# Kernel optimization log

Measured on AMD Instinct MI355X. Metric: run time of the kernel, lower is better.

## Reference

```python
import jax, jax.numpy as jnp
import numpy as np

BLOCK_SIZE = 256
EMB = 384
HEAD = 64
B = 256
T = 256

def setup_inputs() -> dict:
    key = jax.random.key(0)
    k1, k2, k3, k4 = jax.random.split(key, 4)
    x = jax.random.normal(k1, (B, T, EMB), dtype=jnp.float32)
    # torch Linear(no bias) default init ~ U(-1/sqrt(in), 1/sqrt(in)); use scaled normal
    s = 1.0 / np.sqrt(EMB)
    Wq = jax.random.normal(k2, (EMB, HEAD), dtype=jnp.float32) * s
    Wk = jax.random.normal(k3, (EMB, HEAD), dtype=jnp.float32) * s
    Wv = jax.random.normal(k4, (EMB, HEAD), dtype=jnp.float32) * s
    return {"x": x, "Wq": Wq, "Wk": Wk, "Wv": Wv}

def reference(x, Wq, Wk, Wv):
    Bb, Tt, C = x.shape
    q = jnp.einsum('btc,ch->bth', x, Wq)
    k = jnp.einsum('btc,ch->bth', x, Wk)
    v = jnp.einsum('btc,ch->bth', x, Wv)
    # NOTE: source scales by C**-0.5 where C = embedding dim (384), not head_size
    scores = jnp.einsum('bth,bsh->bts', q, k) * (C ** -0.5)  # [B,T,T]
    causal = jnp.tril(jnp.ones((Tt, Tt), dtype=bool))
    scores = jnp.where(causal, scores, -jnp.inf)
    weights = jax.nn.softmax(scores, axis=-1)
    # dropout is identity in eval mode (reference baseline)
    out = jnp.einsum('bts,bsh->bth', weights, v)
    return out
```

## Files before the change

kernel.cpp:

```cpp
#include <hip/hip_runtime.h>
#include <hip/hip_bf16.h>
#include <cstdint>
#include <cstddef>

#define B_DIM 256
#define T_DIM 256
#define EMB   384
#define HEAD  64
#define QS    (B_DIM * T_DIM * HEAD)

typedef __attribute__((ext_vector_type(8))) short bf16x8;
typedef __attribute__((ext_vector_type(4))) float f32x4;
typedef __attribute__((ext_vector_type(4))) unsigned int u32x4;

__device__ __forceinline__ unsigned short f2bf(float f) {
    union { float f; unsigned int u; } v; v.f = f;
    unsigned int r = v.u + 0x7fffu + ((v.u >> 16) & 1u);
    return (unsigned short)(r >> 16);
}

__global__ void wprep_kernel(const float* __restrict__ Wq, const float* __restrict__ Wk,
                             const float* __restrict__ Wv, unsigned short* __restrict__ Wb) {
    int idx = blockIdx.x * blockDim.x + threadIdx.x;
    if (idx >= 192 * EMB) return;
    int n = idx / EMB, k = idx - n * EMB;
    const float* W = (n < 64) ? Wq : (n < 128) ? Wk : Wv;
    Wb[idx] = f2bf(W[k * HEAD + (n & 63)]);
}

__global__ __launch_bounds__(256) void qkv_kernel(const float* __restrict__ x,
                                                  const unsigned short* __restrict__ Wb,
                                                  unsigned short* __restrict__ qkv) {
    __shared__ unsigned short Xs[64][72];
    __shared__ unsigned short Ws[192][72];
    const int tid = threadIdx.x;
    const int w = tid >> 6, lane = tid & 63, qd = lane >> 4, l15 = lane & 15;
    const int m0 = blockIdx.x * 64;

    f32x4 acc[4][3];
#pragma unroll
    for (int mt = 0; mt < 4; ++mt)
#pragma unroll
        for (int nt = 0; nt < 3; ++nt) acc[mt][nt] = (f32x4){0.f, 0.f, 0.f, 0.f};

    for (int kk = 0; kk < EMB; kk += 64) {
#pragma unroll
        for (int s = 0; s < 4; ++s) {
            int i = tid + 256 * s;
            int row = i >> 4, c4 = (i & 15) << 2;
            const float4 vx = *(const float4*)(x + (size_t)(m0 + row) * EMB + kk + c4);
            unsigned int lo = (unsigned)f2bf(vx.x) | ((unsigned)f2bf(vx.y) << 16);
            unsigned int hi = (unsigned)f2bf(vx.z) | ((unsigned)f2bf(vx.w) << 16);
            *(uint2*)&Xs[row][c4] = make_uint2(lo, hi);
        }
#pragma unroll
        for (int s = 0; s < 6; ++s) {
            int i = tid + 256 * s;
            int row = i >> 3, ch = (i & 7) << 3;
            *(u32x4*)&Ws[row][ch] = *(const u32x4*)(Wb + row * EMB + kk + ch);
        }
        __syncthreads();
#pragma unroll
        for (int kb = 0; kb < 2; ++kb) {
            bf16x8 a[4], bb[3];
#pragma unroll
            for (int mt = 0; mt < 4; ++mt)
                a[mt] = *(const bf16x8*)&Xs[16 * mt + l15][32 * kb + 8 * qd];
#pragma unroll
            for (int nt = 0; nt < 3; ++nt)
                bb[nt] = *(const bf16x8*)&Ws[48 * w + 16 * nt + l15][32 * kb + 8 * qd];
#pragma unroll
            for (int mt = 0; mt < 4; ++mt)
#pragma unroll
                for (int nt = 0; nt < 3; ++nt)
                    acc[mt][nt] = __builtin_amdgcn_mfma_f32_16x16x32_bf16(a[mt], bb[nt], acc[mt][nt], 0, 0, 0);
        }
        __syncthreads();
    }
#pragma unroll
    for (int nt = 0; nt < 3; ++nt) {
        int n = 48 * w + 16 * nt + l15;
        int arr = n >> 6, h = n & 63;
        unsigned short* dst = qkv + (size_t)arr * QS + h;
#pragma unroll
        for (int mt = 0; mt < 4; ++mt)
#pragma unroll
            for (int reg = 0; reg < 4; ++reg) {
                int row = m0 + 16 * mt + 4 * qd + reg;
                dst[(size_t)row * HEAD] = f2bf(acc[mt][nt][reg]);
            }
    }
}

__global__ __launch_bounds__(256, 1) void attn_kernel(const unsigned short* __restrict__ qkv,
                                                      float* __restrict__ out) {
    __shared__ unsigned short ks[256][72];
    __shared__ unsigned short vT[64][264];
    __shared__ unsigned short Ps[4][16][72];
    const int tid = threadIdx.x;
    const int w = tid >> 6, lane = tid & 63, qd = lane >> 4, l15 = lane & 15;
    const int b = blockIdx.x;
    const unsigned short* qb = qkv + (size_t)b * T_DIM * HEAD;
    const unsigned short* kb = qkv + (size_t)QS + (size_t)b * T_DIM * HEAD;
    const unsigned short* vb = qkv + 2 * (size_t)QS + (size_t)b * T_DIM * HEAD;

#pragma unroll
    for (int s = 0; s < 8; ++s) {
        int i = tid + 256 * s;
        int row = i >> 3, ch = (i & 7) << 3;
        *(u32x4*)&ks[row][ch] = *(const u32x4*)(kb + row * HEAD + ch);
    }
#pragma unroll
    for (int s = 0; s < 4; ++s) {
        int i = tid + 256 * s;
        int t = i >> 2, d0 = (i & 3) << 4;
        union { u32x4 v; unsigned short u[8]; } t0, t1;
        t0.v = *(const u32x4*)(vb + t * HEAD + d0);
        t1.v = *(const u32x4*)(vb + t * HEAD + d0 + 8);
#pragma unroll
        for (int e = 0; e < 8; ++e) { vT[d0 + e][t] = t0.u[e]; vT[d0 + 8 + e][t] = t1.u[e]; }
    }
    bf16x8 aq[4][2];
#pragma unroll
    for (int mt = 0; mt < 4; ++mt)
#pragma unroll
        for (int kbi = 0; kbi < 2; ++kbi)
            aq[mt][kbi] = *(const bf16x8*)(qb + (64 * mt + 16 * w + l15) * HEAD + 32 * kbi + 8 * qd);
    __syncthreads();

    f32x4 O[4][4];
    float l[4][4];
#pragma unroll
    for (int mt = 0; mt < 4; ++mt)
#pragma unroll
        for (int dn = 0; dn < 4; ++dn) O[mt][dn] = (f32x4){0.f, 0.f, 0.f, 0.f};
#pragma unroll
    for (int mt = 0; mt < 4; ++mt)
#pragma unroll
        for (int reg = 0; reg < 4; ++reg) l[mt][reg] = 0.f;

    const float cExp = 1.4426950408889634f / 19.595917942265423f;

    for (int mt = 0; mt < 4; ++mt) {
        for (int j = 0; j <= mt; ++j) {
            const int ntmax = (j == mt) ? w : 3;
            f32x4 S[4];
#pragma unroll
            for (int nt = 0; nt < 4; ++nt) {
                if (nt <= ntmax) {
                    bf16x8 b0 = *(const bf16x8*)&ks[64 * j + 16 * nt + l15][8 * qd];
                    bf16x8 b1 = *(const bf16x8*)&ks[64 * j + 16 * nt + l15][32 + 8 * qd];
                    f32x4 s = __builtin_amdgcn_mfma_f32_16x16x32_bf16(aq[mt][0], b0, (f32x4){0.f,0.f,0.f,0.f}, 0, 0, 0);
                    s = __builtin_amdgcn_mfma_f32_16x16x32_bf16(aq[mt][1], b1, s, 0, 0, 0);
                    S[nt] = s;
                }
            }
#pragma unroll
            for (int nt = 0; nt < 4; ++nt) {
#pragma unroll
                for (int reg = 0; reg < 4; ++reg) {
                    float p = 0.0f;
                    if (nt <= ntmax) {
                        p = exp2f(S[nt][reg] * cExp);
                        if (j == mt && nt == w && (l15 > 4 * qd + reg)) p = 0.0f;
                    }
                    l[mt][reg] += p;
                    Ps[w][4 * qd + reg][16 * nt + l15] = f2bf(p);
                }
            }
            bf16x8 ap0 = *(const bf16x8*)&Ps[w][l15][8 * qd];
            bf16x8 ap1 = *(const bf16x8*)&Ps[w][l15][32 + 8 * qd];
#pragma unroll
            for (int dn = 0; dn < 4; ++dn) {
                bf16x8 bv0 = *(const bf16x8*)&vT[16 * dn + l15][64 * j + 8 * qd];
                bf16x8 bv1 = *(const bf16x8*)&vT[16 * dn + l15][64 * j + 32 + 8 * qd];
                O[mt][dn] = __builtin_amdgcn_mfma_f32_16x16x32_bf16(ap0, bv0, O[mt][dn], 0, 0, 0);
                O[mt][dn] = __builtin_amdgcn_mfma_f32_16x16x32_bf16(ap1, bv1, O[mt][dn], 0, 0, 0);
            }
        }
    }

#pragma unroll
    for (int mt = 0; mt < 4; ++mt) {
#pragma unroll
        for (int reg = 0; reg < 4; ++reg) {
            float s = l[mt][reg];
            s += __shfl_xor(s, 1);
            s += __shfl_xor(s, 2);
            s += __shfl_xor(s, 4);
            s += __shfl_xor(s, 8);
            float inv = 1.0f / s;
            int row = 64 * mt + 16 * w + 4 * qd + reg;
            float* dst = out + ((size_t)b * T_DIM + row) * HEAD;
#pragma unroll
            for (int dn = 0; dn < 4; ++dn)
                dst[16 * dn + l15] = O[mt][dn][reg] * inv;
        }
    }
}

extern "C" void kernel_launch(void* const* d_in, const int* in_sizes, int n_in,
                              void* d_out, int out_size, void* d_ws, size_t ws_size,
                              hipStream_t stream) {
    const float* x  = (const float*)d_in[0];
    const float* Wq = (const float*)d_in[1];
    const float* Wk = (const float*)d_in[2];
    const float* Wv = (const float*)d_in[3];
    float* out = (float*)d_out;

    unsigned short* qkv = (unsigned short*)d_ws;
    unsigned short* Wb  = qkv + 3 * (size_t)QS;

    wprep_kernel<<<(192 * EMB + 255) / 256, 256, 0, stream>>>(Wq, Wk, Wv, Wb);
    qkv_kernel<<<(B_DIM * T_DIM) / 64, 256, 0, stream>>>(x, Wb, qkv);
    attn_kernel<<<B_DIM, 256, 0, stream>>>(qkv, out);
}
```

Baseline: 194.2 us.

## Enlarge QKV tiles with direct-to-LDS weight loads and balance causal attention across 8 waves

The QKV projection now computes 128 rows per block, with each wave owning a 64x96 output tile. Pre-swizzled bf16 weights are loaded straight into LDS via global_load_lds, and x is converted with a packed bf16 instruction. The attention kernel moves to 512 threads, and each wave handles query tiles w and 15-w so the causal work is balanced across waves. The goal is more reuse per block, fewer conversion instructions and better wave parallelism in attention, at the cost of higher register pressure from 24 accumulators and a new LDS swizzle layout.

```diff
diff --git a/kernel.cpp b/kernel.cpp
--- a/kernel.cpp
+++ b/kernel.cpp
@@ -19,84 +19,104 @@
     return (unsigned short)(r >> 16);
 }
 
+__device__ __forceinline__ unsigned int pkbf(float a, float b) {
+#if __has_builtin(__builtin_amdgcn_cvt_pk_bf16_f32)
+    typedef __attribute__((ext_vector_type(2))) __bf16 bf16x2_t;
+    bf16x2_t r = __builtin_amdgcn_cvt_pk_bf16_f32(a, b);
+    return *(unsigned int*)&r;
+#else
+    return (unsigned)f2bf(a) | ((unsigned)f2bf(b) << 16);
+#endif
+}
+
 __global__ void wprep_kernel(const float* __restrict__ Wq, const float* __restrict__ Wk,
                              const float* __restrict__ Wv, unsigned short* __restrict__ Wb) {
-    int idx = blockIdx.x * blockDim.x + threadIdx.x;
-    if (idx >= 192 * EMB) return;
-    int n = idx / EMB, k = idx - n * EMB;
-    const float* W = (n < 64) ? Wq : (n < 128) ? Wk : Wv;
-    Wb[idx] = f2bf(W[k * HEAD + (n & 63)]);
+    int g = blockIdx.x * blockDim.x + threadIdx.x;
+    if (g >= 9216) return;
+    int kkstep = g / 1536, rem = g - kkstep * 1536;
+    int r = rem >> 3, cs = rem & 7, c = cs ^ (r & 7);
+    const float* W = (r < 64) ? Wq : (r < 128) ? Wk : Wv;
+    int h = r & 63;
+#pragma unroll
+    for (int e = 0; e < 8; ++e) {
+        int k = kkstep * 64 + c * 8 + e;
+        Wb[(size_t)g * 8 + e] = f2bf(W[k * HEAD + h]);
+    }
 }
 
 __global__ __launch_bounds__(256) void qkv_kernel(const float* __restrict__ x,
                                                   const unsigned short* __restrict__ Wb,
                                                   unsigned short* __restrict__ qkv) {
-    __shared__ unsigned short Xs[64][72];
-    __shared__ unsigned short Ws[192][72];
+    __shared__ unsigned short Xs[128][72];
+    __shared__ unsigned short Ws[192 * 64];
     const int tid = threadIdx.x;
     const int w = tid >> 6, lane = tid & 63, qd = lane >> 4, l15 = lane & 15;
-    const int m0 = blockIdx.x * 64;
-
-    f32x4 acc[4][3];
+    const int mh = w >> 1, nh = w & 1;
+    const int m0 = blockIdx.x * 128;
+
+    f32x4 acc[4][6];
 #pragma unroll
     for (int mt = 0; mt < 4; ++mt)
 #pragma unroll
-        for (int nt = 0; nt < 3; ++nt) acc[mt][nt] = (f32x4){0.f, 0.f, 0.f, 0.f};
-
-    for (int kk = 0; kk < EMB; kk += 64) {
-#pragma unroll
-        for (int s = 0; s < 4; ++s) {
+        for (int nt = 0; nt < 6; ++nt) acc[mt][nt] = (f32x4){0.f, 0.f, 0.f, 0.f};
+
+    for (int kk = 0; kk < 6; ++kk) {
+#pragma unroll
+        for (int s = 0; s < 6; ++s) {
+            int idx = s * 256 + w * 64;
+            const unsigned short* gp = Wb + (size_t)(kk * 1536 + idx + lane) * 8;
+            unsigned short* lp = Ws + (size_t)idx * 8;
+            __builtin_amdgcn_global_load_lds(
+                (const __attribute__((address_space(1))) unsigned int*)gp,
+                (__attribute__((address_space(3))) unsigned int*)lp, 16, 0, 0);
+        }
+#pragma unroll
+        for (int s = 0; s < 8; ++s) {
             int i = tid + 256 * s;
             int row = i >> 4, c4 = (i & 15) << 2;
-            const float4 vx = *(const float4*)(x + (size_t)(m0 + row) * EMB + kk + c4);
-            unsigned int lo = (unsigned)f2bf(vx.x) | ((unsigned)f2bf(vx.y) << 16);
-            unsigned int hi = (unsigned)f2bf(vx.z) | ((unsigned)f2bf(vx.w) << 16);
-            *(uint2*)&Xs[row][c4] = make_uint2(lo, hi);
-        }
-#pragma unroll
-        for (int s = 0; s < 6; ++s) {
-            int i = tid + 256 * s;
-            int row = i >> 3, ch = (i & 7) << 3;
-            *(u32x4*)&Ws[row][ch] = *(const u32x4*)(Wb + row * EMB + kk + ch);
+            const float4 vx = *(const float4*)(x + (size_t)(m0 + row) * EMB + kk * 64 + c4);
+            *(uint2*)&Xs[row][c4] = make_uint2(pkbf(vx.x, vx.y), pkbf(vx.z, vx.w));
         }
         __syncthreads();
 #pragma unroll
         for (int kb = 0; kb < 2; ++kb) {
-            bf16x8 a[4], bb[3];
+            bf16x8 a[4], bb[6];
 #pragma unroll
             for (int mt = 0; mt < 4; ++mt)
-                a[mt] = *(const bf16x8*)&Xs[16 * mt + l15][32 * kb + 8 * qd];
-#pragma unroll
-            for (int nt = 0; nt < 3; ++nt)
-                bb[nt] = *(const bf16x8*)&Ws[48 * w + 16 * nt + l15][32 * kb + 8 * qd];
+                a[mt] = *(const bf16x8*)&Xs[64 * mh + 16 * mt + l15][32 * kb + 8 * qd];
+#pragma unroll
+            for (int nt = 0; nt < 6; ++nt) {
+                int n = 96 * nh + 16 * nt + l15;
+                bb[nt] = *(const bf16x8*)&Ws[n * 64 + (((4 * kb + qd) ^ (n & 7)) << 3)];
+            }
 #pragma unroll
             for (int mt = 0; mt < 4; ++mt)
 #pragma unroll
-                for (int nt = 0; nt < 3; ++nt)
+                for (int nt = 0; nt < 6; ++nt)
                     acc[mt][nt] = __builtin_amdgcn_mfma_f32_16x16x32_bf16(a[mt], bb[nt], acc[mt][nt], 0, 0, 0);
         }
         __syncthreads();
     }
 #pragma unroll
-    for (int nt = 0; nt < 3; ++nt) {
-        int n = 48 * w + 16 * nt + l15;
+    for (int nt = 0; nt < 6; ++nt) {
+        int n = 96 * nh + 16 * nt + l15;
         int arr = n >> 6, h = n & 63;
         unsigned short* dst = qkv + (size_t)arr * QS + h;
 #pragma unroll
         for (int mt = 0; mt < 4; ++mt)
 #pragma unroll
             for (int reg = 0; reg < 4; ++reg) {
-                int row = m0 + 16 * mt + 4 * qd + reg;
+                int row = m0 + 64 * mh + 16 * mt + 4 * qd + reg;
                 dst[(size_t)row * HEAD] = f2bf(acc[mt][nt][reg]);
             }
     }
 }
 
-__global__ __launch_bounds__(256, 1) void attn_kernel(const unsigned short* __restrict__ qkv,
+__global__ __launch_bounds__(512, 1) void attn_kernel(const unsigned short* __restrict__ qkv,
                                                       float* __restrict__ out) {
     __shared__ unsigned short ks[256][72];
     __shared__ unsigned short vT[64][264];
-    __shared__ unsigned short Ps[4][16][72];
+    __shared__ unsigned short Ps[8][16][72];
     const int tid = threadIdx.x;
     const int w = tid >> 6, lane = tid & 63, qd = lane >> 4, l15 = lane & 15;
     const int b = blockIdx.x;
@@ -105,14 +125,14 @@
     const unsigned short* vb = qkv + 2 * (size_t)QS + (size_t)b * T_DIM * HEAD;
 
 #pragma unroll
-    for (int s = 0; s < 8; ++s) {
-        int i = tid + 256 * s;
+    for (int s = 0; s < 4; ++s) {
+        int i = tid + 512 * s;
         int row = i >> 3, ch = (i & 7) << 3;
         *(u32x4*)&ks[row][ch] = *(const u32x4*)(kb + row * HEAD + ch);
     }
 #pragma unroll
-    for (int s = 0; s < 4; ++s) {
-        int i = tid + 256 * s;
+    for (int s = 0; s < 2; ++s) {
+        int i = tid + 512 * s;
         int t = i >> 2, d0 = (i & 3) << 4;
         union { u32x4 v; unsigned short u[8]; } t0, t1;
         t0.v = *(const u32x4*)(vb + t * HEAD + d0);
@@ -120,38 +140,40 @@
 #pragma unroll
         for (int e = 0; e < 8; ++e) { vT[d0 + e][t] = t0.u[e]; vT[d0 + 8 + e][t] = t1.u[e]; }
     }
-    bf16x8 aq[4][2];
-#pragma unroll
-    for (int mt = 0; mt < 4; ++mt)
+    const int tiles[2] = { w, 15 - w };
+    bf16x8 aq[2][2];
+#pragma unroll
+    for (int ti = 0; ti < 2; ++ti)
 #pragma unroll
         for (int kbi = 0; kbi < 2; ++kbi)
-            aq[mt][kbi] = *(const bf16x8*)(qb + (64 * mt + 16 * w + l15) * HEAD + 32 * kbi + 8 * qd);
+            aq[ti][kbi] = *(const bf16x8*)(qb + (16 * tiles[ti] + l15) * HEAD + 32 * kbi + 8 * qd);
     __syncthreads();
 
-    f32x4 O[4][4];
-    float l[4][4];
-#pragma unroll
-    for (int mt = 0; mt < 4; ++mt)
-#pragma unroll
-        for (int dn = 0; dn < 4; ++dn) O[mt][dn] = (f32x4){0.f, 0.f, 0.f, 0.f};
-#pragma unroll
-    for (int mt = 0; mt < 4; ++mt)
-#pragma unroll
-        for (int reg = 0; reg < 4; ++reg) l[mt][reg] = 0.f;
+    f32x4 O[2][4];
+    float l[2][4];
+#pragma unroll
+    for (int ti = 0; ti < 2; ++ti) {
+#pragma unroll
+        for (int dn = 0; dn < 4; ++dn) O[ti][dn] = (f32x4){0.f, 0.f, 0.f, 0.f};
+#pragma unroll
+        for (int reg = 0; reg < 4; ++reg) l[ti][reg] = 0.f;
+    }
 
     const float cExp = 1.4426950408889634f / 19.595917942265423f;
 
-    for (int mt = 0; mt < 4; ++mt) {
-        for (int j = 0; j <= mt; ++j) {
-            const int ntmax = (j == mt) ? w : 3;
+#pragma unroll
+    for (int ti = 0; ti < 2; ++ti) {
+        const int t = tiles[ti];
+        for (int jc = 0; jc <= (t >> 2); ++jc) {
+            const int ntmax = min(3, t - 4 * jc);
             f32x4 S[4];
 #pragma unroll
             for (int nt = 0; nt < 4; ++nt) {
                 if (nt <= ntmax) {
-                    bf16x8 b0 = *(const bf16x8*)&ks[64 * j + 16 * nt + l15][8 * qd];
-                    bf16x8 b1 = *(const bf16x8*)&ks[64 * j + 16 * nt + l15][32 + 8 * qd];
-                    f32x4 s = __builtin_amdgcn_mfma_f32_16x16x32_bf16(aq[mt][0], b0, (f32x4){0.f,0.f,0.f,0.f}, 0, 0, 0);
-                    s = __builtin_amdgcn_mfma_f32_16x16x32_bf16(aq[mt][1], b1, s, 0, 0, 0);
+                    bf16x8 b0 = *(const bf16x8*)&ks[64 * jc + 16 * nt + l15][8 * qd];
+                    bf16x8 b1 = *(const bf16x8*)&ks[64 * jc + 16 * nt + l15][32 + 8 * qd];
+                    f32x4 s = __builtin_amdgcn_mfma_f32_16x16x32_bf16(aq[ti][0], b0, (f32x4){0.f,0.f,0.f,0.f}, 0, 0, 0);
+                    s = __builtin_amdgcn_mfma_f32_16x16x32_bf16(aq[ti][1], b1, s, 0, 0, 0);
                     S[nt] = s;
                 }
             }
@@ -162,9 +184,9 @@
                     float p = 0.0f;
                     if (nt <= ntmax) {
                         p = exp2f(S[nt][reg] * cExp);
-                        if (j == mt && nt == w && (l15 > 4 * qd + reg)) p = 0.0f;
+                        if (4 * jc + nt == t && (l15 > 4 * qd + reg)) p = 0.0f;
                     }
-                    l[mt][reg] += p;
+                    l[ti][reg] += p;
                     Ps[w][4 * qd + reg][16 * nt + l15] = f2bf(p);
                 }
             }
@@ -172,29 +194,29 @@
             bf16x8 ap1 = *(const bf16x8*)&Ps[w][l15][32 + 8 * qd];
 #pragma unroll
             for (int dn = 0; dn < 4; ++dn) {
-                bf16x8 bv0 = *(const bf16x8*)&vT[16 * dn + l15][64 * j + 8 * qd];
-                bf16x8 bv1 = *(const bf16x8*)&vT[16 * dn + l15][64 * j + 32 + 8 * qd];
-                O[mt][dn] = __builtin_amdgcn_mfma_f32_16x16x32_bf16(ap0, bv0, O[mt][dn], 0, 0, 0);
-                O[mt][dn] = __builtin_amdgcn_mfma_f32_16x16x32_bf16(ap1, bv1, O[mt][dn], 0, 0, 0);
-            }
-        }
-    }
-
-#pragma unroll
-    for (int mt = 0; mt < 4; ++mt) {
+                bf16x8 bv0 = *(const bf16x8*)&vT[16 * dn + l15][64 * jc + 8 * qd];
+                bf16x8 bv1 = *(const bf16x8*)&vT[16 * dn + l15][64 * jc + 32 + 8 * qd];
+                O[ti][dn] = __builtin_amdgcn_mfma_f32_16x16x32_bf16(ap0, bv0, O[ti][dn], 0, 0, 0);
+                O[ti][dn] = __builtin_amdgcn_mfma_f32_16x16x32_bf16(ap1, bv1, O[ti][dn], 0, 0, 0);
+            }
+        }
+    }
+
+#pragma unroll
+    for (int ti = 0; ti < 2; ++ti) {
 #pragma unroll
         for (int reg = 0; reg < 4; ++reg) {
-            float s = l[mt][reg];
+            float s = l[ti][reg];
             s += __shfl_xor(s, 1);
             s += __shfl_xor(s, 2);
             s += __shfl_xor(s, 4);
             s += __shfl_xor(s, 8);
             float inv = 1.0f / s;
-            int row = 64 * mt + 16 * w + 4 * qd + reg;
+            int row = 16 * tiles[ti] + 4 * qd + reg;
             float* dst = out + ((size_t)b * T_DIM + row) * HEAD;
 #pragma unroll
             for (int dn = 0; dn < 4; ++dn)
-                dst[16 * dn + l15] = O[mt][dn][reg] * inv;
+                dst[16 * dn + l15] = O[ti][dn][reg] * inv;
         }
     }
 }
@@ -211,7 +233,7 @@
     unsigned short* qkv = (unsigned short*)d_ws;
     unsigned short* Wb  = qkv + 3 * (size_t)QS;
 
-    wprep_kernel<<<(192 * EMB + 255) / 256, 256, 0, stream>>>(Wq, Wk, Wv, Wb);
-    qkv_kernel<<<(B_DIM * T_DIM) / 64, 256, 0, stream>>>(x, Wb, qkv);
-    attn_kernel<<<B_DIM, 256, 0, stream>>>(qkv, out);
-}
+    wprep_kernel<<<36, 256, 0, stream>>>(Wq, Wk, Wv, Wb);
+    qkv_kernel<<<(B_DIM * T_DIM) / 128, 256, 0, stream>>>(x, Wb, qkv);
+    attn_kernel<<<B_DIM, 512, 0, stream>>>(qkv, out);
+}
```

New measurement: 184.1 us. 1.06x faster.
